# Performance work log

Hardware: AMD Instinct MI355X
Metric: run time of the kernel (lower is better)

Reference implementation:

```python
import jax, jax.numpy as jnp
import numpy as np

EPS = 1e-8  # torch.nn.CosineSimilarity eps


def setup_inputs() -> dict:
    key = jax.random.key(0)
    k1, k2, k3 = jax.random.split(key, 3)
    C, S, D = 1024, 16, 512
    x = jax.random.normal(k1, (C, S, D), dtype=jnp.float32)
    w = jax.random.normal(k2, (1,), dtype=jnp.float32)
    b = jax.random.normal(k3, (1,), dtype=jnp.float32)
    return {"x": x, "w": w, "b": b}


def reference(x, w, b):
    # stable_ge2e: leave-one-out positive centroids, full negative centroids.
    C, S, D = x.shape
    wp = jax.nn.softplus(w)  # (1,)

    sum_c = x.sum(axis=1)                      # (C, D)
    mean_c = sum_c / S                         # negative centroids (C, D)
    loo = (sum_c[:, None, :] - x) / (S - 1.0)  # leave-one-out centroids (C, S, D)

    nx = jnp.linalg.norm(x, axis=-1)           # (C, S)
    nmean = jnp.linalg.norm(mean_c, axis=-1)   # (C,)
    nloo = jnp.linalg.norm(loo, axis=-1)       # (C, S)

    # cosine similarities (clamped denominator, as in torch CosineSimilarity)
    sim_neg = jnp.einsum('jid,kd->jik', x, mean_c) / jnp.maximum(
        nx[:, :, None] * nmean[None, None, :], EPS)          # (C, S, C)
    sim_pos = jnp.einsum('jid,jid->ji', x, loo) / jnp.maximum(nx * nloo, EPS)  # (C, S)

    # on the diagonal k == j use the leave-one-out positive centroid
    eye = jnp.eye(C, dtype=bool)
    sim = jnp.where(eye[:, None, :], sim_pos[:, :, None], sim_neg)  # (C, S, C)

    logits = wp * sim + b
    logS = jax.nn.log_softmax(logits, axis=-1)
    Sji_j = jnp.einsum('jij->ji', logS)                        # (C, S) diagonal
    Sji_k = jax.scipy.special.logsumexp(logS, axis=-1)         # (C, S) (== 0 post-softmax)
    loss = -(Sji_j - Sji_k).reshape(-1)
    return loss.mean()
```

## Files before the change

### kernel.cpp

```cpp
#include <hip/hip_runtime.h>
#include <math.h>

#define CC 1024
#define SS 16
#define DD 512
#define RR (CC*SS)
#define EPSV 1e-8f
#define LDB 520

typedef __attribute__((ext_vector_type(8))) short short8;
typedef __attribute__((ext_vector_type(4))) float f32x4;
typedef unsigned short ushort_t;

__device__ __forceinline__ unsigned short f2bf(float f) {
  unsigned u = __float_as_uint(f);
  u += 0x7fffu + ((u >> 16) & 1u);
  return (unsigned short)(u >> 16);
}

__device__ __forceinline__ void async16(void* l, const void* g) {
  __builtin_amdgcn_global_load_lds(
      (const __attribute__((address_space(1))) void*)g,
      (__attribute__((address_space(3))) void*)l, 16, 0, 0);
}

__device__ __forceinline__ float softplusf(float v) {
  return (v > 20.f) ? v : log1pf(expf(v));
}

__global__ __launch_bounds__(256) void k_pre(
    const float* __restrict__ x, ushort_t* __restrict__ mn,
    float* __restrict__ nx, float* __restrict__ simpos,
    ushort_t* __restrict__ xn) {
  __shared__ float xs[SS * DD];
  __shared__ float sums[DD];
  __shared__ float red[4];
  __shared__ float snm;
  __shared__ float rinv[SS];
  const int j = blockIdx.x, tid = threadIdx.x;
  const float4* xj = (const float4*)(x + (size_t)j * SS * DD);
  float4* xs4 = (float4*)xs;
  for (int i = tid; i < SS * DD / 4; i += 256) xs4[i] = xj[i];
  __syncthreads();
  float m2 = 0.f;
  for (int d = tid; d < DD; d += 256) {
    float s = 0.f;
#pragma unroll
    for (int i = 0; i < SS; ++i) s += xs[i * DD + d];
    sums[d] = s;
    float m = s * (1.0f / SS);
    m2 += m * m;
  }
#pragma unroll
  for (int off = 32; off > 0; off >>= 1) m2 += __shfl_xor(m2, off, 64);
  const int wid = tid >> 6, lane = tid & 63;
  if (lane == 0) red[wid] = m2;
  __syncthreads();
  if (tid == 0) snm = sqrtf(red[0] + red[1] + red[2] + red[3]);
  __syncthreads();
  const float inm = (1.0f / SS) / snm;
  for (int d = tid; d < DD; d += 256)
    mn[(size_t)j * DD + d] = f2bf(sums[d] * inm);
  for (int i = wid; i < SS; i += 4) {
    float nx2 = 0.f, dxs = 0.f, t2 = 0.f;
    for (int d = lane; d < DD; d += 64) {
      float xv = xs[i * DD + d];
      float sc = sums[d];
      nx2 = fmaf(xv, xv, nx2);
      dxs = fmaf(xv, sc, dxs);
      float tv = sc - xv;
      t2 = fmaf(tv, tv, t2);
    }
#pragma unroll
    for (int off = 32; off > 0; off >>= 1) {
      nx2 += __shfl_xor(nx2, off, 64);
      dxs += __shfl_xor(dxs, off, 64);
      t2  += __shfl_xor(t2,  off, 64);
    }
    if (lane == 0) {
      float nxv = sqrtf(nx2);
      float tn  = sqrtf(t2);
      float num = (dxs - nx2) * (1.0f / (SS - 1));
      float den = fmaxf(nxv * tn * (1.0f / (SS - 1)), EPSV);
      nx[j * SS + i] = nxv;
      rinv[i] = 1.0f / nxv;
      simpos[j * SS + i] = num / den;
    }
  }
  __syncthreads();
  if (xn) {
    unsigned* dst = (unsigned*)(xn + (size_t)j * SS * DD);
    for (int idx = tid; idx < SS * DD / 2; idx += 256) {
      const int e = idx * 2;
      const float ri = rinv[e >> 9];
      unsigned lo = f2bf(xs[e] * ri);
      unsigned hi = f2bf(xs[e + 1] * ri);
      dst[idx] = lo | (hi << 16);
    }
  }
}

template <bool USE_XN>
__global__ __launch_bounds__(256) void k_gemm(
    const float* __restrict__ x, const ushort_t* __restrict__ xn,
    const ushort_t* __restrict__ mn, const float* __restrict__ nx,
    const float* __restrict__ simpos, const float* __restrict__ wptr,
    const float* __restrict__ bptr, float* __restrict__ ps) {
  __shared__ ushort_t bs[2][64 * LDB];
  const int tid = threadIdx.x;
  const int wid = tid >> 6, lane = tid & 63;
  const int cL = lane & 15, quad = lane >> 4;
  const int rb = (int)blockIdx.x >> 1, cb = (int)blockIdx.x & 1;
  const int r0 = rb * 128, cbase = cb * 512;
  const float wp = softplusf(wptr[0]), bv = bptr[0];

  short8 af[2][16];
  int jw[2];
  float sp[2][4], sacc[2][4];
#pragma unroll
  for (int rt = 0; rt < 2; ++rt) {
    const int row = r0 + wid * 32 + rt * 16 + cL;
    if (USE_XN) {
      const short8* src = (const short8*)(xn + (size_t)row * DD);
#pragma unroll
      for (int kc = 0; kc < 16; ++kc) af[rt][kc] = src[kc * 4 + quad];
    } else {
      const float* xr = x + (size_t)row * DD;
      const float invn = 1.0f / nx[row];
#pragma unroll
      for (int kc = 0; kc < 16; ++kc) {
        const int k0 = kc * 32 + quad * 8;
        float4 p = *(const float4*)(xr + k0);
        float4 q = *(const float4*)(xr + k0 + 4);
        short8 v;
        v[0] = f2bf(p.x * invn); v[1] = f2bf(p.y * invn);
        v[2] = f2bf(p.z * invn); v[3] = f2bf(p.w * invn);
        v[4] = f2bf(q.x * invn); v[5] = f2bf(q.y * invn);
        v[6] = f2bf(q.z * invn); v[7] = f2bf(q.w * invn);
        af[rt][kc] = v;
      }
    }
    jw[rt] = (r0 + wid * 32 + rt * 16) >> 4;
#pragma unroll
    for (int r = 0; r < 4; ++r) {
      sp[rt][r] = simpos[r0 + wid * 32 + rt * 16 + quad * 4 + r];
      sacc[rt][r] = 0.f;
    }
  }

  {
    const ushort_t* gsrc = mn + (size_t)cbase * DD;
#pragma unroll
    for (int t = 0; t < 16; ++t) {
      const int rr = wid + t * 4;
      async16(&bs[0][rr * LDB + lane * 8], gsrc + (size_t)rr * DD + lane * 8);
    }
  }
  __syncthreads();

  for (int cc = 0; cc < 8; ++cc) {
    if (cc < 7) {
      const ushort_t* gsrc = mn + (size_t)(cbase + (cc + 1) * 64) * DD;
      ushort_t* dst = bs[(cc + 1) & 1];
#pragma unroll
      for (int t = 0; t < 16; ++t) {
        const int rr = wid + t * 4;
        async16(&dst[rr * LDB + lane * 8], gsrc + (size_t)rr * DD + lane * 8);
      }
    }
    const ushort_t* B = bs[cc & 1];
    f32x4 acc[2][4];
#pragma unroll
    for (int rt = 0; rt < 2; ++rt)
#pragma unroll
      for (int f = 0; f < 4; ++f) acc[rt][f] = (f32x4){0.f, 0.f, 0.f, 0.f};
#pragma unroll
    for (int kc = 0; kc < 16; ++kc) {
      short8 bfr[4];
#pragma unroll
      for (int f = 0; f < 4; ++f)
        bfr[f] = *(const short8*)&B[(f * 16 + cL) * LDB + kc * 32 + quad * 8];
#pragma unroll
      for (int rt = 0; rt < 2; ++rt)
#pragma unroll
        for (int f = 0; f < 4; ++f)
          acc[rt][f] = __builtin_amdgcn_mfma_f32_16x16x32_bf16(
              af[rt][kc], bfr[f], acc[rt][f], 0, 0, 0);
    }
    const int c0 = cbase + cc * 64;
#pragma unroll
    for (int rt = 0; rt < 2; ++rt)
#pragma unroll
      for (int f = 0; f < 4; ++f) {
        const int cg = c0 + f * 16 + cL;
        const bool diag = (cg == jw[rt]);
#pragma unroll
        for (int r = 0; r < 4; ++r) {
          const float sim = diag ? sp[rt][r] : acc[rt][f][r];
          sacc[rt][r] += __expf(fmaf(wp, sim, bv));
        }
      }
    __syncthreads();
  }

#pragma unroll
  for (int rt = 0; rt < 2; ++rt)
#pragma unroll
    for (int r = 0; r < 4; ++r) {
      float v = sacc[rt][r];
#pragma unroll
      for (int off = 1; off < 16; off <<= 1) v += __shfl_xor(v, off, 64);
      if (cL == 0)
        ps[(size_t)(r0 + wid * 32 + rt * 16 + quad * 4 + r) * 2 + cb] = v;
    }
}

__global__ __launch_bounds__(256) void k_combine(
    const float* __restrict__ ps, const float* __restrict__ simpos,
    const float* __restrict__ wptr, const float* __restrict__ bptr,
    float* __restrict__ p2) {
  __shared__ float red[4];
  const int tid = threadIdx.x;
  const int row = blockIdx.x * 256 + tid;
  const float wp = softplusf(wptr[0]), bv = bptr[0];
  const float s = ps[row * 2] + ps[row * 2 + 1];
  float v = logf(s) - fmaf(wp, simpos[row], bv);
#pragma unroll
  for (int off = 32; off > 0; off >>= 1) v += __shfl_xor(v, off, 64);
  if ((tid & 63) == 0) red[tid >> 6] = v;
  __syncthreads();
  if (tid == 0) p2[blockIdx.x] = red[0] + red[1] + red[2] + red[3];
}

__global__ __launch_bounds__(64) void k_fin(const float* __restrict__ p2,
                                            float* __restrict__ out) {
  const int tid = threadIdx.x;
  float v = p2[tid];
#pragma unroll
  for (int off = 32; off > 0; off >>= 1) v += __shfl_xor(v, off, 64);
  if (tid == 0) out[0] = v * (1.0f / RR);
}

extern "C" void kernel_launch(void* const* d_in, const int* in_sizes, int n_in,
                              void* d_out, int out_size, void* d_ws, size_t ws_size,
                              hipStream_t stream) {
  const float* x = (const float*)d_in[0];
  const float* w = (const float*)d_in[1];
  const float* b = (const float*)d_in[2];
  float* out = (float*)d_out;

  const size_t xn_bytes = (size_t)RR * DD * 2;
  const size_t rest = (size_t)CC * DD * 2 + (size_t)RR * 4 * 2 +
                      (size_t)RR * 2 * 4 + 64 * 4;
  const bool use_xn = ws_size >= xn_bytes + rest + 256;

  char* base = (char*)d_ws;
  ushort_t* xn = use_xn ? (ushort_t*)base : nullptr;
  char* p = base + (use_xn ? xn_bytes : 0);
  ushort_t* mn = (ushort_t*)p;  p += (size_t)CC * DD * 2;
  float* nx     = (float*)p;    p += (size_t)RR * 4;
  float* simpos = (float*)p;    p += (size_t)RR * 4;
  float* ps     = (float*)p;    p += (size_t)RR * 2 * 4;
  float* p2     = (float*)p;

  k_pre<<<CC, 256, 0, stream>>>(x, mn, nx, simpos, xn);
  if (use_xn)
    k_gemm<true><<<256, 256, 0, stream>>>(x, xn, mn, nx, simpos, w, b, ps);
  else
    k_gemm<false><<<256, 256, 0, stream>>>(x, xn, mn, nx, simpos, w, b, ps);
  k_combine<<<RR / 256, 256, 0, stream>>>(ps, simpos, w, b, p2);
  k_fin<<<1, 64, 0, stream>>>(p2, out);
}
```

Measured before the change: 113.3 us.

## Split GEMM columns four ways, vectorize preprocessing, merge loss reduction kernels

The GEMM grid doubles from 256 to 512 blocks. Each block now covers 256 columns in 32-column chunks instead of 512 columns in 64-column chunks, and a swizzled tile mapping spreads neighbouring blocks across row tiles. The aim is to fill more of the machine's CUs, with half the LDS per block and a launch bound that permits two blocks per CU. The preprocessing kernel switches to float2/float4 vectorized LDS access and packed bf16 stores. The combine and final-reduce kernels are merged into one single-block 1024-thread kernel to cut a launch, at the cost of doing the final reduction serially in one block.

```diff
diff --git a/kernel.cpp b/kernel.cpp
--- a/kernel.cpp
+++ b/kernel.cpp
@@ -7,6 +7,7 @@
 #define RR (CC*SS)
 #define EPSV 1e-8f
 #define LDB 520
+#define CHUNK 32
 
 typedef __attribute__((ext_vector_type(8))) short short8;
 typedef __attribute__((ext_vector_type(4))) float f32x4;
@@ -38,38 +39,47 @@
   __shared__ float snm;
   __shared__ float rinv[SS];
   const int j = blockIdx.x, tid = threadIdx.x;
+  const int wid = tid >> 6, lane = tid & 63;
   const float4* xj = (const float4*)(x + (size_t)j * SS * DD);
   float4* xs4 = (float4*)xs;
-  for (int i = tid; i < SS * DD / 4; i += 256) xs4[i] = xj[i];
-  __syncthreads();
-  float m2 = 0.f;
-  for (int d = tid; d < DD; d += 256) {
-    float s = 0.f;
-#pragma unroll
-    for (int i = 0; i < SS; ++i) s += xs[i * DD + d];
-    sums[d] = s;
-    float m = s * (1.0f / SS);
-    m2 += m * m;
-  }
+#pragma unroll
+  for (int t = 0; t < 8; ++t) xs4[tid + t * 256] = xj[tid + t * 256];
+  __syncthreads();
+
+  float sx = 0.f, sy = 0.f;
+  const float2* xs2 = (const float2*)xs;
+#pragma unroll
+  for (int i = 0; i < SS; ++i) {
+    float2 v = xs2[i * (DD / 2) + tid];
+    sx += v.x; sy += v.y;
+  }
+  ((float2*)sums)[tid] = make_float2(sx, sy);
+  const float mxs = sx * (1.0f / SS), mys = sy * (1.0f / SS);
+  float m2 = mxs * mxs + mys * mys;
 #pragma unroll
   for (int off = 32; off > 0; off >>= 1) m2 += __shfl_xor(m2, off, 64);
-  const int wid = tid >> 6, lane = tid & 63;
   if (lane == 0) red[wid] = m2;
   __syncthreads();
   if (tid == 0) snm = sqrtf(red[0] + red[1] + red[2] + red[3]);
   __syncthreads();
   const float inm = (1.0f / SS) / snm;
-  for (int d = tid; d < DD; d += 256)
-    mn[(size_t)j * DD + d] = f2bf(sums[d] * inm);
+  {
+    unsigned lo = f2bf(sx * inm), hi = f2bf(sy * inm);
+    ((unsigned*)(mn + (size_t)j * DD))[tid] = lo | (hi << 16);
+  }
+
   for (int i = wid; i < SS; i += 4) {
     float nx2 = 0.f, dxs = 0.f, t2 = 0.f;
-    for (int d = lane; d < DD; d += 64) {
-      float xv = xs[i * DD + d];
-      float sc = sums[d];
-      nx2 = fmaf(xv, xv, nx2);
-      dxs = fmaf(xv, sc, dxs);
-      float tv = sc - xv;
-      t2 = fmaf(tv, tv, t2);
+    const float2* xr2 = (const float2*)(xs + i * DD);
+    const float2* sm2 = (const float2*)sums;
+#pragma unroll
+    for (int d2 = 0; d2 < DD / 2; d2 += 64) {
+      float2 xv = xr2[d2 + lane];
+      float2 sc = sm2[d2 + lane];
+      nx2 = fmaf(xv.x, xv.x, fmaf(xv.y, xv.y, nx2));
+      dxs = fmaf(xv.x, sc.x, fmaf(xv.y, sc.y, dxs));
+      float tx = sc.x - xv.x, ty = sc.y - xv.y;
+      t2 = fmaf(tx, tx, fmaf(ty, ty, t2));
     }
 #pragma unroll
     for (int off = 32; off > 0; off >>= 1) {
@@ -89,29 +99,35 @@
   }
   __syncthreads();
   if (xn) {
-    unsigned* dst = (unsigned*)(xn + (size_t)j * SS * DD);
-    for (int idx = tid; idx < SS * DD / 2; idx += 256) {
-      const int e = idx * 2;
-      const float ri = rinv[e >> 9];
-      unsigned lo = f2bf(xs[e] * ri);
-      unsigned hi = f2bf(xs[e + 1] * ri);
-      dst[idx] = lo | (hi << 16);
+    uint2* dst = (uint2*)(xn + (size_t)j * SS * DD);
+    const float4* src4 = (const float4*)xs;
+#pragma unroll
+    for (int t = 0; t < 8; ++t) {
+      const int idx = tid + t * 256;
+      const float ri = rinv[idx >> 7];
+      float4 v = src4[idx];
+      uint2 o;
+      o.x = (unsigned)f2bf(v.x * ri) | ((unsigned)f2bf(v.y * ri) << 16);
+      o.y = (unsigned)f2bf(v.z * ri) | ((unsigned)f2bf(v.w * ri) << 16);
+      dst[idx] = o;
     }
   }
 }
 
 template <bool USE_XN>
-__global__ __launch_bounds__(256) void k_gemm(
+__global__ __launch_bounds__(256, 2) void k_gemm(
     const float* __restrict__ x, const ushort_t* __restrict__ xn,
     const ushort_t* __restrict__ mn, const float* __restrict__ nx,
     const float* __restrict__ simpos, const float* __restrict__ wptr,
     const float* __restrict__ bptr, float* __restrict__ ps) {
-  __shared__ ushort_t bs[2][64 * LDB];
+  __shared__ ushort_t bs[2][CHUNK * LDB];
   const int tid = threadIdx.x;
   const int wid = tid >> 6, lane = tid & 63;
   const int cL = lane & 15, quad = lane >> 4;
-  const int rb = (int)blockIdx.x >> 1, cb = (int)blockIdx.x & 1;
-  const int r0 = rb * 128, cbase = cb * 512;
+  const int bid = (int)blockIdx.x;
+  const int tile = (bid & 7) * 64 + (bid >> 3);
+  const int rb = tile >> 2, cb = tile & 3;
+  const int r0 = rb * 128, cbase = cb * 256;
   const float wp = softplusf(wptr[0]), bv = bptr[0];
 
   short8 af[2][16];
@@ -151,7 +167,7 @@
   {
     const ushort_t* gsrc = mn + (size_t)cbase * DD;
 #pragma unroll
-    for (int t = 0; t < 16; ++t) {
+    for (int t = 0; t < 8; ++t) {
       const int rr = wid + t * 4;
       async16(&bs[0][rr * LDB + lane * 8], gsrc + (size_t)rr * DD + lane * 8);
     }
@@ -160,38 +176,38 @@
 
   for (int cc = 0; cc < 8; ++cc) {
     if (cc < 7) {
-      const ushort_t* gsrc = mn + (size_t)(cbase + (cc + 1) * 64) * DD;
+      const ushort_t* gsrc = mn + (size_t)(cbase + (cc + 1) * CHUNK) * DD;
       ushort_t* dst = bs[(cc + 1) & 1];
 #pragma unroll
-      for (int t = 0; t < 16; ++t) {
+      for (int t = 0; t < 8; ++t) {
         const int rr = wid + t * 4;
         async16(&dst[rr * LDB + lane * 8], gsrc + (size_t)rr * DD + lane * 8);
       }
     }
     const ushort_t* B = bs[cc & 1];
-    f32x4 acc[2][4];
+    f32x4 acc[2][2];
 #pragma unroll
     for (int rt = 0; rt < 2; ++rt)
 #pragma unroll
-      for (int f = 0; f < 4; ++f) acc[rt][f] = (f32x4){0.f, 0.f, 0.f, 0.f};
+      for (int f = 0; f < 2; ++f) acc[rt][f] = (f32x4){0.f, 0.f, 0.f, 0.f};
 #pragma unroll
     for (int kc = 0; kc < 16; ++kc) {
-      short8 bfr[4];
-#pragma unroll
-      for (int f = 0; f < 4; ++f)
+      short8 bfr[2];
+#pragma unroll
+      for (int f = 0; f < 2; ++f)
         bfr[f] = *(const short8*)&B[(f * 16 + cL) * LDB + kc * 32 + quad * 8];
 #pragma unroll
       for (int rt = 0; rt < 2; ++rt)
 #pragma unroll
-        for (int f = 0; f < 4; ++f)
+        for (int f = 0; f < 2; ++f)
           acc[rt][f] = __builtin_amdgcn_mfma_f32_16x16x32_bf16(
               af[rt][kc], bfr[f], acc[rt][f], 0, 0, 0);
     }
-    const int c0 = cbase + cc * 64;
+    const int c0 = cbase + cc * CHUNK;
 #pragma unroll
     for (int rt = 0; rt < 2; ++rt)
 #pragma unroll
-      for (int f = 0; f < 4; ++f) {
+      for (int f = 0; f < 2; ++f) {
         const int cg = c0 + f * 16 + cL;
         const bool diag = (cg == jw[rt]);
 #pragma unroll
@@ -211,34 +227,35 @@
 #pragma unroll
       for (int off = 1; off < 16; off <<= 1) v += __shfl_xor(v, off, 64);
       if (cL == 0)
-        ps[(size_t)(r0 + wid * 32 + rt * 16 + quad * 4 + r) * 2 + cb] = v;
-    }
-}
-
-__global__ __launch_bounds__(256) void k_combine(
+        ps[(size_t)(r0 + wid * 32 + rt * 16 + quad * 4 + r) * 4 + cb] = v;
+    }
+}
+
+__global__ __launch_bounds__(1024) void k_loss(
     const float* __restrict__ ps, const float* __restrict__ simpos,
     const float* __restrict__ wptr, const float* __restrict__ bptr,
-    float* __restrict__ p2) {
-  __shared__ float red[4];
+    float* __restrict__ out) {
+  __shared__ float red[16];
   const int tid = threadIdx.x;
-  const int row = blockIdx.x * 256 + tid;
   const float wp = softplusf(wptr[0]), bv = bptr[0];
-  const float s = ps[row * 2] + ps[row * 2 + 1];
-  float v = logf(s) - fmaf(wp, simpos[row], bv);
-#pragma unroll
-  for (int off = 32; off > 0; off >>= 1) v += __shfl_xor(v, off, 64);
-  if ((tid & 63) == 0) red[tid >> 6] = v;
-  __syncthreads();
-  if (tid == 0) p2[blockIdx.x] = red[0] + red[1] + red[2] + red[3];
-}
-
-__global__ __launch_bounds__(64) void k_fin(const float* __restrict__ p2,
-                                            float* __restrict__ out) {
-  const int tid = threadIdx.x;
-  float v = p2[tid];
-#pragma unroll
-  for (int off = 32; off > 0; off >>= 1) v += __shfl_xor(v, off, 64);
-  if (tid == 0) out[0] = v * (1.0f / RR);
+  float acc = 0.f;
+#pragma unroll
+  for (int i = 0; i < RR / 1024; ++i) {
+    const int row = i * 1024 + tid;
+    const f32x4 v = ((const f32x4*)ps)[row];
+    const float s = v[0] + v[1] + v[2] + v[3];
+    acc += logf(s) - fmaf(wp, simpos[row], bv);
+  }
+#pragma unroll
+  for (int off = 32; off > 0; off >>= 1) acc += __shfl_xor(acc, off, 64);
+  if ((tid & 63) == 0) red[tid >> 6] = acc;
+  __syncthreads();
+  if (tid < 64) {
+    float v = (tid < 16) ? red[tid] : 0.f;
+#pragma unroll
+    for (int off = 8; off > 0; off >>= 1) v += __shfl_xor(v, off, 64);
+    if (tid == 0) out[0] = v * (1.0f / RR);
+  }
 }
 
 extern "C" void kernel_launch(void* const* d_in, const int* in_sizes, int n_in,
@@ -251,7 +268,7 @@
 
   const size_t xn_bytes = (size_t)RR * DD * 2;
   const size_t rest = (size_t)CC * DD * 2 + (size_t)RR * 4 * 2 +
-                      (size_t)RR * 2 * 4 + 64 * 4;
+                      (size_t)RR * 4 * 4;
   const bool use_xn = ws_size >= xn_bytes + rest + 256;
 
   char* base = (char*)d_ws;
@@ -260,14 +277,12 @@
   ushort_t* mn = (ushort_t*)p;  p += (size_t)CC * DD * 2;
   float* nx     = (float*)p;    p += (size_t)RR * 4;
   float* simpos = (float*)p;    p += (size_t)RR * 4;
-  float* ps     = (float*)p;    p += (size_t)RR * 2 * 4;
-  float* p2     = (float*)p;
+  float* ps     = (float*)p;
 
   k_pre<<<CC, 256, 0, stream>>>(x, mn, nx, simpos, xn);
   if (use_xn)
-    k_gemm<true><<<256, 256, 0, stream>>>(x, xn, mn, nx, simpos, w, b, ps);
+    k_gemm<true><<<512, 256, 0, stream>>>(x, xn, mn, nx, simpos, w, b, ps);
   else
-    k_gemm<false><<<256, 256, 0, stream>>>(x, xn, mn, nx, simpos, w, b, ps);
-  k_combine<<<RR / 256, 256, 0, stream>>>(ps, simpos, w, b, p2);
-  k_fin<<<1, 64, 0, stream>>>(p2, out);
-}
+    k_gemm<false><<<512, 256, 0, stream>>>(x, xn, mn, nx, simpos, w, b, ps);
+  k_loss<<<1, 1024, 0, stream>>>(ps, simpos, w, b, out);
+}
```

Result: no change. 113.5 us (+0.2%).
